# Kernel tuning notes

Measured on AMD Instinct MI355X. Metric: run time of the kernel, lower is better.

## Reference

```python
import jax, jax.numpy as jnp
import numpy as np

B, NB, BS, C, H = 4, 128, 128, 256, 8  # batch, num_blocks, block_size, dim, heads


def setup_inputs() -> dict:
    key = jax.random.key(0)
    ks = jax.random.split(key, 8)
    x = jax.random.normal(ks[0], (B, NB * BS, C), dtype=jnp.float32)
    attn_mask = jax.random.randint(ks[1], (NB, BS, BS + 1), 0, 2, dtype=jnp.int32)
    # guarantee the global-node column is always attendable (avoids all--inf rows)
    attn_mask = attn_mask.at[:, :, BS].set(1)
    edge_feats = jax.random.normal(ks[2], (NB, BS, BS + 1, 4), dtype=jnp.float32)
    w_qkv = jax.random.normal(ks[3], (C, 3 * C), dtype=jnp.float32) * (C ** -0.5)
    b_qkv = jnp.zeros((3 * C,), dtype=jnp.float32)
    w_proj = jax.random.normal(ks[4], (C, C), dtype=jnp.float32) * (C ** -0.5)
    b_proj = jnp.zeros((C,), dtype=jnp.float32)
    w_gate = jax.random.normal(ks[5], (4, H), dtype=jnp.float32) * 0.01  # nn.init.normal_(std=0.01)
    b_gate = jnp.zeros((H,), dtype=jnp.float32)
    return {"x": x, "attn_mask": attn_mask, "edge_feats": edge_feats,
            "w_qkv": w_qkv, "b_qkv": b_qkv, "w_proj": w_proj, "b_proj": b_proj,
            "w_gate": w_gate, "b_gate": b_gate}


def reference(x, attn_mask, edge_feats, w_qkv, b_qkv, w_proj, b_proj, w_gate, b_gate):
    Bv, N, Cv = x.shape
    nb, bs, _ = attn_mask.shape
    Hv = b_gate.shape[0]
    hd = Cv // Hv
    scale = hd ** -0.5

    x_blk = x.reshape(Bv, nb, bs, Cv)
    block_node = x_blk.mean(axis=2, keepdims=True)           # [B, nb, 1, C]
    kv = jnp.concatenate([x_blk, block_node], axis=2)        # [B, nb, bs+1, C]

    qkv_q = x_blk @ w_qkv + b_qkv
    qkv_kv = kv @ w_qkv + b_qkv
    q = qkv_q[..., :Cv].reshape(Bv, nb, bs, Hv, hd)
    k = qkv_kv[..., Cv:2 * Cv].reshape(Bv, nb, bs + 1, Hv, hd)
    v = qkv_kv[..., 2 * Cv:].reshape(Bv, nb, bs + 1, Hv, hd)

    scores = jnp.einsum('bnqhd,bnkhd->bnqkh', q, k) * scale  # [B, nb, bs, bs+1, H]

    # physics bias: zero out (with channel-3 = 1) at the global-node column and the diagonal
    qi = jnp.arange(bs)[:, None]
    ki = jnp.arange(bs + 1)[None, :]
    special = (ki == bs) | (ki == qi)                        # [bs, bs+1]
    special_vec = jnp.array([0.0, 0.0, 0.0, 1.0], dtype=x.dtype)
    bias = jnp.where(special[:, :, None], special_vec, edge_feats[..., :4])  # [nb, bs, bs+1, 4]
    bias = jnp.broadcast_to(bias[None], (Bv, nb, bs, bs + 1, 4))

    scores = scores + bias[..., 3:4]
    mask = (attn_mask[None, :, :, :, None] != 0)             # [1, nb, bs, bs+1, 1]
    scores = jnp.where(mask, scores, -jnp.inf)
    probs = jax.nn.softmax(scores, axis=3)

    gate = jnp.where(mask, bias @ w_gate + b_gate, jnp.zeros((), dtype=x.dtype))
    combined = probs + gate                                  # [B, nb, bs, bs+1, H]

    out = jnp.einsum('bnqkh,bnkhd->bnqhd', combined, v).reshape(Bv, N, Cv)
    return out @ w_proj + b_proj
```

## Files before the change

### kernel.cpp

```cpp
#include <hip/hip_runtime.h>

#define B_   4
#define NB_  128
#define BS_  128
#define C_   256
#define H_   8
#define KL_  129
#define SC2_   0.25503486f
#define LOG2E_ 1.4426950408889634f
#define RSTR_  99072

typedef unsigned short u16;
typedef unsigned int   u32;
typedef short          s16;
typedef __attribute__((ext_vector_type(8))) __bf16 bf16x8;
typedef __attribute__((ext_vector_type(4))) float  f32x4;

__device__ __forceinline__ float bf16tof(u16 u) {
  union { u32 i; float f; } v; v.i = ((u32)u) << 16; return v.f;
}
__device__ __forceinline__ u16 fbits(float a) {
  union { __bf16 h; u16 u; } v; v.h = (__bf16)a; return v.u;
}
__device__ __forceinline__ u32 pk2(float a, float b) {
  union { __bf16 h[2]; u32 u; } v;
  v.h[0] = (__bf16)a; v.h[1] = (__bf16)b;
  return v.u;
}
__device__ __forceinline__ float asf(u32 u) {
  union { u32 i; float f; } v; v.i = u; return v.f;
}

__device__ __forceinline__ void glds16(const void* g, void* l) {
  __builtin_amdgcn_global_load_lds(
      (const __attribute__((address_space(1))) unsigned int*)g,
      (__attribute__((address_space(3))) unsigned int*)l, 16, 0, 0);
}

__global__ __launch_bounds__(256) void meancvt_kernel(const float* __restrict__ x,
                                                      u16* __restrict__ xb) {
  const int blk = blockIdx.x;
  const int c = threadIdx.x;
  const float* p = x + (size_t)blk * BS_ * C_ + c;
  u16* q = xb + (size_t)blk * (KL_ * C_) + c;
  float s = 0.f;
  #pragma unroll 4
  for (int r = 0; r < BS_; ++r) {
    const float v = p[(size_t)r * C_];
    s += v;
    q[(size_t)r * C_] = fbits(v);
  }
  q[(size_t)BS_ * C_] = fbits(s * (1.0f / BS_));
}

__global__ __launch_bounds__(256) void wt_kernel(const float* __restrict__ wq,
      const float* __restrict__ wp, s16* __restrict__ wtq, s16* __restrict__ wtp) {
  const int i = blockIdx.x * 256 + threadIdx.x;
  if (i < 768 * 256) {
    const int nn = i >> 8, k = i & 255;
    wtq[i] = (s16)fbits(wq[k * 768 + nn]);
  } else {
    const int j = i - 768 * 256;
    const int nn = j >> 8, k = j & 255;
    wtp[j] = (s16)fbits(wp[k * 256 + nn]);
  }
}

__global__ __launch_bounds__(256) void pre_kernel(const int* __restrict__ mask,
      const float* __restrict__ ef, const float* __restrict__ wg_,
      const float* __restrict__ bg, u16* __restrict__ g4t,
      u16* __restrict__ s4t) {
  const int t = blockIdx.x * 256 + threadIdx.x;
  const int kq = t & 31;
  const int row = t >> 5;
  const int n = row >> 7;
  const int q = row & 127;
  const int key0 = kq * 4;
  const int* mrow = mask + (size_t)row * KL_;
  const float* erow = ef + (size_t)row * KL_ * 4;
  float e0[4], e1[4], e2[4], e3[4];
  int m[4];
  #pragma unroll
  for (int r = 0; r < 4; ++r) {
    const int key = key0 + r;
    m[r] = mrow[key];
    float4 ev = *(const float4*)(erow + (size_t)key * 4);
    if (key == q) { ev.x = 0.f; ev.y = 0.f; ev.z = 0.f; ev.w = 1.f; }
    e0[r] = ev.x; e1[r] = ev.y; e2[r] = ev.z; e3[r] = ev.w;
  }
  float s[4];
  #pragma unroll
  for (int r = 0; r < 4; ++r) s[r] = m[r] ? e3[r] * LOG2E_ : -1e30f;
  *(uint2*)(s4t + (size_t)row * 128 + key0) =
      uint2{pk2(s[0], s[1]), pk2(s[2], s[3])};
  #pragma unroll
  for (int h = 0; h < 8; ++h) {
    const float w0 = wg_[h], w1 = wg_[8 + h], w2 = wg_[16 + h],
                w3 = wg_[24 + h], bh = bg[h];
    float gt[4];
    #pragma unroll
    for (int r = 0; r < 4; ++r) {
      const float gg = fmaf(e0[r], w0, fmaf(e1[r], w1,
                        fmaf(e2[r], w2, fmaf(e3[r], w3, bh))));
      gt[r] = m[r] ? gg : 0.f;
    }
    *(uint2*)(g4t + (((size_t)n * 8 + h) * 128 + q) * 128 + key0) =
        uint2{pk2(gt[0], gt[1]), pk2(gt[2], gt[3])};
  }
}

template<bool STRIDED, bool OBF16, int NS>
__global__ __launch_bounds__(256) void mfma_gemm(const s16* __restrict__ Ab,
      const s16* __restrict__ Bt, const float* __restrict__ bias,
      void* __restrict__ outv) {
  __shared__ __align__(16) s16 Al[2][128 * 64];
  __shared__ __align__(16) s16 Bl[2][128 * 64];
  const int tid = threadIdx.x;
  const int lane = tid & 63;
  const int wid = tid >> 6;
  constexpr int ncol = NS / 128;
  const int per  = gridDim.x >> 3;
  const int gidx = (blockIdx.x & 7) * per + (blockIdx.x >> 3);
  const int arow = gidx / ncol;
  const int col0 = (gidx - arow * ncol) * 128;
  const int row0 = arow * 128;
  const int ldrow = lane >> 3;
  const int lcb   = (lane & 7) * 16;

  auto STAGE = [&](int k0, int buf) {
    #pragma unroll
    for (int j = 0; j < 4; ++j) {
      const int c = wid * 4 + j;
      const int row = c * 8 + ldrow;
      const int scb = lcb ^ ((row & 7) << 4);
      glds16(Bt + (size_t)(col0 + row) * C_ + k0 + (scb >> 1), &Bl[buf][c * 512]);
    }
    #pragma unroll
    for (int j = 0; j < 4; ++j) {
      const int c = wid * 4 + j;
      const int row = c * 8 + ldrow;
      const int scb = lcb ^ ((row & 7) << 4);
      if constexpr (STRIDED)
        glds16(Ab + (size_t)arow * RSTR_ + (size_t)row * 768 + 256
                  + k0 + (scb >> 1), &Al[buf][c * 512]);
      else
        glds16(Ab + (size_t)(row0 + row) * C_ + k0 + (scb >> 1), &Al[buf][c * 512]);
    }
  };

  f32x4 acc[4][4];
  #pragma unroll
  for (int i = 0; i < 4; ++i)
    #pragma unroll
    for (int j = 0; j < 4; ++j) acc[i][j] = f32x4{0.f, 0.f, 0.f, 0.f};

  STAGE(0, 0);
  __syncthreads();

  const int fr = lane & 15;
  const int ar0 = (wid >> 1) * 64;
  const int ac0 = (wid & 1) * 64;
  #pragma unroll 1
  for (int t = 0; t < 4; ++t) {
    if (t < 3) STAGE((t + 1) * 64, (t + 1) & 1);
    const char* Ac = (const char*)&Al[t & 1][0];
    const char* Bc = (const char*)&Bl[t & 1][0];
    #pragma unroll
    for (int kk = 0; kk < 64; kk += 32) {
      const int kb = kk * 2 + (lane >> 4) * 16;
      bf16x8 af[4], bfr[4];
      #pragma unroll
      for (int mf = 0; mf < 4; ++mf) {
        const int row = ar0 + mf * 16 + fr;
        af[mf] = *(const bf16x8*)(Ac + row * 128 + (kb ^ ((row & 7) << 4)));
      }
      #pragma unroll
      for (int nf = 0; nf < 4; ++nf) {
        const int row = ac0 + nf * 16 + fr;
        bfr[nf] = *(const bf16x8*)(Bc + row * 128 + (kb ^ ((row & 7) << 4)));
      }
      #pragma unroll
      for (int mf = 0; mf < 4; ++mf)
        #pragma unroll
        for (int nf = 0; nf < 4; ++nf)
          acc[mf][nf] = __builtin_amdgcn_mfma_f32_16x16x32_bf16(
              af[mf], bfr[nf], acc[mf][nf], 0, 0, 0);
    }
    __syncthreads();
  }

  const int orow0 = row0 + (wid >> 1) * 64 + (lane >> 4) * 4;
  const int ocol0 = col0 + (wid & 1) * 64 + (lane & 15);
  #pragma unroll
  for (int nf = 0; nf < 4; ++nf) {
    const int col = ocol0 + nf * 16;
    const float bb = bias[col];
    #pragma unroll
    for (int mf = 0; mf < 4; ++mf) {
      #pragma unroll
      for (int r = 0; r < 4; ++r) {
        const size_t row = (size_t)(orow0 + mf * 16 + r);
        const float v = acc[mf][nf][r] + bb;
        if constexpr (OBF16) ((u16*)outv)[row * NS + col] = fbits(v);
        else                 ((float*)outv)[row * NS + col] = v;
      }
    }
  }
}

__global__ __launch_bounds__(256, 4) void attn_kernel(u16* __restrict__ qkv,
      const u16* __restrict__ g4t, const u16* __restrict__ s4t,
      const float* __restrict__ wg_, const float* __restrict__ bg) {
  __shared__ __align__(16) char lds[36176];
  const int bid = blockIdx.x;
  const int xcd = bid & 7;
  const int j   = bid >> 3;
  const int wgi = xcd * 64 + (j >> 3);
  const int h   = j & 7;
  const int n = wgi & (NB_ - 1);
  const int tid = threadIdx.x;
  const int wid = tid >> 6, lane = tid & 63;
  const int g = lane >> 4, ql = lane & 15;
  u16*  Kl = (u16*)lds;
  u16*  vt = (u16*)(lds + 10320);
  char* pb = lds + 18768 + wid * 4352;

  u16* qkv_blk = qkv + (size_t)wgi * RSTR_;
  const u16* sbase = s4t + (size_t)n * (128 * 128);
  const u16* gbase = g4t + ((size_t)n * 8 + h) * (128 * 128);

  for (int i = tid; i < 516; i += 256) {
    const int r = i >> 2, dc = i & 3;
    const uint4 u = *(const uint4*)(qkv_blk + (size_t)r * 768 + 256 + h * 32 + dc * 8);
    *(uint4*)(Kl + r * 40 + dc * 8) = u;
  }
  for (int i = tid; i < 512; i += 256) {
    const int r = i >> 2, dc = i & 3;
    const uint4 u = *(const uint4*)(qkv_blk + (size_t)r * 768 + 512 + h * 32 + dc * 8);
    u16* col = vt + (dc * 8) * 132 + r;
    col[0 * 132] = (u16)(u.x & 0xffff); col[1 * 132] = (u16)(u.x >> 16);
    col[2 * 132] = (u16)(u.y & 0xffff); col[3 * 132] = (u16)(u.y >> 16);
    col[4 * 132] = (u16)(u.z & 0xffff); col[5 * 132] = (u16)(u.z >> 16);
    col[6 * 132] = (u16)(u.w & 0xffff); col[7 * 132] = (u16)(u.w >> 16);
  }
  __syncthreads();

  const float v128a = bf16tof(qkv_blk[(size_t)128 * 768 + 512 + h * 32 + ql]);
  const float v128b = bf16tof(qkv_blk[(size_t)128 * 768 + 512 + h * 32 + 16 + ql]);
  const float gk128 = wg_[24 + h] + bg[h];

  #pragma unroll 1
  for (int mi = 0; mi < 2; ++mi) {
    const int mt = wid * 2 + mi;
    const int qrow = mt * 16 + ql;
    const bf16x8 qf = *(const bf16x8*)(qkv_blk + (size_t)qrow * 768 + h * 32 + g * 8);
    const u16* srow = sbase + (size_t)qrow * 128;
    const u16* grow = gbase + (size_t)qrow * 128;

    float psum = 0.f;
    uint2 gab[8];
    #pragma unroll
    for (int f = 0; f < 8; ++f) {
      const bf16x8 kf = *(const bf16x8*)(Kl + (16 * f + ql) * 40 + 8 * g);
      f32x4 st = __builtin_amdgcn_mfma_f32_16x16x32_bf16(
          kf, qf, f32x4{0.f, 0.f, 0.f, 0.f}, 0, 0, 0);
      const uint2 sv = *(const uint2*)(srow + 16 * f + 4 * g);
      gab[f] = *(const uint2*)(grow + 16 * f + 4 * g);
      float w[4];
      w[0] = __builtin_amdgcn_exp2f(fmaf(st[0], SC2_, asf(sv.x << 16)));
      w[1] = __builtin_amdgcn_exp2f(fmaf(st[1], SC2_, asf(sv.x & 0xffff0000u)));
      w[2] = __builtin_amdgcn_exp2f(fmaf(st[2], SC2_, asf(sv.y << 16)));
      w[3] = __builtin_amdgcn_exp2f(fmaf(st[3], SC2_, asf(sv.y & 0xffff0000u)));
      psum += (w[0] + w[1]) + (w[2] + w[3]);
      *(uint2*)(pb + ql * 272 + (16 * f + 4 * g) * 2) =
          uint2{pk2(w[0], w[1]), pk2(w[2], w[3])};
    }
    const bf16x8 kf8 = *(const bf16x8*)(Kl + 128 * 40 + 8 * g);
    f32x4 st8 = __builtin_amdgcn_mfma_f32_16x16x32_bf16(
        kf8, qf, f32x4{0.f, 0.f, 0.f, 0.f}, 0, 0, 0);
    const float w0 = __builtin_amdgcn_exp2f(
        fmaf(st8[0], SC2_, (g == 0) ? LOG2E_ : -1e30f));
    psum += w0;
    psum += __shfl_xor(psum, 16);
    psum += __shfl_xor(psum, 32);
    const float inv = __builtin_amdgcn_rcpf(psum);
    const float c128 = fmaf(w0, inv, (g == 0) ? gk128 : 0.f);

    f32x4 ow0{0.f,0.f,0.f,0.f}, ow1{0.f,0.f,0.f,0.f};
    #pragma unroll
    for (int c = 0; c < 4; ++c) {
      const bf16x8 pa = *(const bf16x8*)(pb + ql * 272 + (32 * c + 8 * g) * 2);
      const bf16x8 v0 = *(const bf16x8*)(vt + ql * 132 + 32 * c + 8 * g);
      const bf16x8 v1 = *(const bf16x8*)(vt + (16 + ql) * 132 + 32 * c + 8 * g);
      ow0 = __builtin_amdgcn_mfma_f32_16x16x32_bf16(pa, v0, ow0, 0, 0, 0);
      ow1 = __builtin_amdgcn_mfma_f32_16x16x32_bf16(pa, v1, ow1, 0, 0, 0);
    }
    #pragma unroll
    for (int f = 0; f < 8; ++f)
      *(uint2*)(pb + ql * 272 + (16 * f + 4 * g) * 2) = gab[f];
    f32x4 og0{0.f,0.f,0.f,0.f}, og1{0.f,0.f,0.f,0.f};
    #pragma unroll
    for (int c = 0; c < 4; ++c) {
      const bf16x8 pa = *(const bf16x8*)(pb + ql * 272 + (32 * c + 8 * g) * 2);
      const bf16x8 v0 = *(const bf16x8*)(vt + ql * 132 + 32 * c + 8 * g);
      const bf16x8 v1 = *(const bf16x8*)(vt + (16 + ql) * 132 + 32 * c + 8 * g);
      og0 = __builtin_amdgcn_mfma_f32_16x16x32_bf16(pa, v0, og0, 0, 0, 0);
      og1 = __builtin_amdgcn_mfma_f32_16x16x32_bf16(pa, v1, og1, 0, 0, 0);
    }
    u16* aop = qkv_blk + (size_t)(mt * 16 + g * 4) * 768 + 256 + h * 32 + ql;
    #pragma unroll
    for (int r = 0; r < 4; ++r) {
      const float iv = __shfl(inv,  4 * g + r);
      const float cc = __shfl(c128, 4 * g + r);
      aop[(size_t)r * 768]      = fbits(fmaf(cc, v128a, fmaf(ow0[r], iv, og0[r])));
      aop[(size_t)r * 768 + 16] = fbits(fmaf(cc, v128b, fmaf(ow1[r], iv, og1[r])));
    }
  }
}

extern "C" void kernel_launch(void* const* d_in, const int* in_sizes, int n_in,
                              void* d_out, int out_size, void* d_ws, size_t ws_size,
                              hipStream_t stream) {
  (void)in_sizes; (void)n_in; (void)out_size; (void)ws_size;
  const float* x      = (const float*)d_in[0];
  const int*   mask   = (const int*)  d_in[1];
  const float* ef     = (const float*)d_in[2];
  const float* w_qkv  = (const float*)d_in[3];
  const float* b_qkv  = (const float*)d_in[4];
  const float* w_proj = (const float*)d_in[5];
  const float* b_proj = (const float*)d_in[6];
  const float* w_gate = (const float*)d_in[7];
  const float* b_gate = (const float*)d_in[8];
  float* out = (float*)d_out;
  char* ws = (char*)d_ws;

  u16* qkv = (u16*)(ws);
  s16* wtq = (s16*)(ws + 101449728);
  s16* wtp = (s16*)(ws + 101842944);
  u16* xb  = (u16*)(ws + 101974016);
  u16* g4t = (u16*)(ws + 101974016);
  u16* s4t = (u16*)d_out;

  meancvt_kernel<<<B_ * NB_, 256, 0, stream>>>(x, xb);
  wt_kernel<<<(768 * 256 + 256 * 256) / 256, 256, 0, stream>>>(
      w_qkv, w_proj, wtq, wtp);
  mfma_gemm<false, true, 768>
      <<<(B_ * NB_ * KL_ / 128) * 6, 256, 0, stream>>>(
      (const s16*)xb, wtq, b_qkv, qkv);
  pre_kernel<<<(NB_ * BS_ * 32) / 256, 256, 0, stream>>>(
      mask, ef, w_gate, b_gate, g4t, s4t);
  attn_kernel<<<B_ * NB_ * H_, 256, 0, stream>>>(
      qkv, (const u16*)g4t, (const u16*)s4t, w_gate, b_gate);
  mfma_gemm<true, false, 256>
      <<<(B_ * NB_ * BS_ / 128) * 2, 256, 0, stream>>>(
      (const s16*)qkv, wtp, b_proj, out);
}
```

Before: 190.9 us.

## Load K fragments from global into registers, drop K LDS staging, raise occupancy

The attention kernel no longer stages K into shared memory. Each wave loads its nine K fragments straight from global memory into registers, which cuts LDS use from about 36 KB to about 26 KB and lets the launch bound ask for 8 blocks per CU. The gate-row loads move to just before use rather than being held in registers across the first MFMA pass, and the attention output is now written over the Q slot instead of the K slot, with the projection GEMM's strided A offset changed to match. The trade-off is redundant global or L2 reads of K by every wave and more register pressure from the kf array, in exchange for higher occupancy.

```diff
diff --git a/kernel.cpp b/kernel.cpp
--- a/kernel.cpp
+++ b/kernel.cpp
@@ -141,7 +141,7 @@
       const int row = c * 8 + ldrow;
       const int scb = lcb ^ ((row & 7) << 4);
       if constexpr (STRIDED)
-        glds16(Ab + (size_t)arow * RSTR_ + (size_t)row * 768 + 256
+        glds16(Ab + (size_t)arow * RSTR_ + (size_t)row * 768
                   + k0 + (scb >> 1), &Al[buf][c * 512]);
       else
         glds16(Ab + (size_t)(row0 + row) * C_ + k0 + (scb >> 1), &Al[buf][c * 512]);
@@ -208,10 +208,10 @@
   }
 }
 
-__global__ __launch_bounds__(256, 4) void attn_kernel(u16* __restrict__ qkv,
+__global__ __launch_bounds__(256, 8) void attn_kernel(u16* __restrict__ qkv,
       const u16* __restrict__ g4t, const u16* __restrict__ s4t,
       const float* __restrict__ wg_, const float* __restrict__ bg) {
-  __shared__ __align__(16) char lds[36176];
+  __shared__ __align__(16) char lds[25856];
   const int bid = blockIdx.x;
   const int xcd = bid & 7;
   const int j   = bid >> 3;
@@ -221,19 +221,13 @@
   const int tid = threadIdx.x;
   const int wid = tid >> 6, lane = tid & 63;
   const int g = lane >> 4, ql = lane & 15;
-  u16*  Kl = (u16*)lds;
-  u16*  vt = (u16*)(lds + 10320);
-  char* pb = lds + 18768 + wid * 4352;
+  u16*  vt = (u16*)lds;
+  char* pb = lds + 8448 + wid * 4352;
 
   u16* qkv_blk = qkv + (size_t)wgi * RSTR_;
   const u16* sbase = s4t + (size_t)n * (128 * 128);
   const u16* gbase = g4t + ((size_t)n * 8 + h) * (128 * 128);
 
-  for (int i = tid; i < 516; i += 256) {
-    const int r = i >> 2, dc = i & 3;
-    const uint4 u = *(const uint4*)(qkv_blk + (size_t)r * 768 + 256 + h * 32 + dc * 8);
-    *(uint4*)(Kl + r * 40 + dc * 8) = u;
-  }
   for (int i = tid; i < 512; i += 256) {
     const int r = i >> 2, dc = i & 3;
     const uint4 u = *(const uint4*)(qkv_blk + (size_t)r * 768 + 512 + h * 32 + dc * 8);
@@ -243,11 +237,10 @@
     col[4 * 132] = (u16)(u.z & 0xffff); col[5 * 132] = (u16)(u.z >> 16);
     col[6 * 132] = (u16)(u.w & 0xffff); col[7 * 132] = (u16)(u.w >> 16);
   }
-  __syncthreads();
-
   const float v128a = bf16tof(qkv_blk[(size_t)128 * 768 + 512 + h * 32 + ql]);
   const float v128b = bf16tof(qkv_blk[(size_t)128 * 768 + 512 + h * 32 + 16 + ql]);
   const float gk128 = wg_[24 + h] + bg[h];
+  __syncthreads();
 
   #pragma unroll 1
   for (int mi = 0; mi < 2; ++mi) {
@@ -257,15 +250,19 @@
     const u16* srow = sbase + (size_t)qrow * 128;
     const u16* grow = gbase + (size_t)qrow * 128;
 
+    bf16x8 kf[9];
+    #pragma unroll
+    for (int f = 0; f < 9; ++f) {
+      int kr = 16 * f + ql; if (kr > 128) kr = 128;
+      kf[f] = *(const bf16x8*)(qkv_blk + (size_t)kr * 768 + 256 + h * 32 + g * 8);
+    }
+
     float psum = 0.f;
-    uint2 gab[8];
     #pragma unroll
     for (int f = 0; f < 8; ++f) {
-      const bf16x8 kf = *(const bf16x8*)(Kl + (16 * f + ql) * 40 + 8 * g);
       f32x4 st = __builtin_amdgcn_mfma_f32_16x16x32_bf16(
-          kf, qf, f32x4{0.f, 0.f, 0.f, 0.f}, 0, 0, 0);
+          kf[f], qf, f32x4{0.f, 0.f, 0.f, 0.f}, 0, 0, 0);
       const uint2 sv = *(const uint2*)(srow + 16 * f + 4 * g);
-      gab[f] = *(const uint2*)(grow + 16 * f + 4 * g);
       float w[4];
       w[0] = __builtin_amdgcn_exp2f(fmaf(st[0], SC2_, asf(sv.x << 16)));
       w[1] = __builtin_amdgcn_exp2f(fmaf(st[1], SC2_, asf(sv.x & 0xffff0000u)));
@@ -275,9 +272,8 @@
       *(uint2*)(pb + ql * 272 + (16 * f + 4 * g) * 2) =
           uint2{pk2(w[0], w[1]), pk2(w[2], w[3])};
     }
-    const bf16x8 kf8 = *(const bf16x8*)(Kl + 128 * 40 + 8 * g);
     f32x4 st8 = __builtin_amdgcn_mfma_f32_16x16x32_bf16(
-        kf8, qf, f32x4{0.f, 0.f, 0.f, 0.f}, 0, 0, 0);
+        kf[8], qf, f32x4{0.f, 0.f, 0.f, 0.f}, 0, 0, 0);
     const float w0 = __builtin_amdgcn_exp2f(
         fmaf(st8[0], SC2_, (g == 0) ? LOG2E_ : -1e30f));
     psum += w0;
@@ -296,8 +292,10 @@
       ow1 = __builtin_amdgcn_mfma_f32_16x16x32_bf16(pa, v1, ow1, 0, 0, 0);
     }
     #pragma unroll
-    for (int f = 0; f < 8; ++f)
-      *(uint2*)(pb + ql * 272 + (16 * f + 4 * g) * 2) = gab[f];
+    for (int f = 0; f < 8; ++f) {
+      const uint2 gv = *(const uint2*)(grow + 16 * f + 4 * g);
+      *(uint2*)(pb + ql * 272 + (16 * f + 4 * g) * 2) = gv;
+    }
     f32x4 og0{0.f,0.f,0.f,0.f}, og1{0.f,0.f,0.f,0.f};
     #pragma unroll
     for (int c = 0; c < 4; ++c) {
@@ -307,7 +305,7 @@
       og0 = __builtin_amdgcn_mfma_f32_16x16x32_bf16(pa, v0, og0, 0, 0, 0);
       og1 = __builtin_amdgcn_mfma_f32_16x16x32_bf16(pa, v1, og1, 0, 0, 0);
     }
-    u16* aop = qkv_blk + (size_t)(mt * 16 + g * 4) * 768 + 256 + h * 32 + ql;
+    u16* aop = qkv_blk + (size_t)(mt * 16 + g * 4) * 768 + h * 32 + ql;
     #pragma unroll
     for (int r = 0; r < 4; ++r) {
       const float iv = __shfl(inv,  4 * g + r);
```

Result: slower. 216.7 us (+13.5%).
